# Kernel optimization log

Hardware: AMD Instinct MI355X
Metric: run time of the kernel (lower is better)

Reference implementation:

```python
import jax, jax.numpy as jnp
import numpy as np

NUM_HEADS = 8
MASK_RATE = 0.5


def setup_inputs() -> dict:
    key = jax.random.key(0)
    ks = jax.random.split(key, 6)
    B, N, C = 8, 1024, 256
    TABLE = 10
    att_embedding = jax.random.normal(ks[0], (B, N, C), dtype=jnp.float32)
    relation_position = jax.random.randint(ks[1], (B, N, N), 0, TABLE, dtype=jnp.int32)
    rel_len = jax.random.randint(ks[2], (B,), 0, 20, dtype=jnp.int32)
    W_qkv = jax.random.normal(ks[3], (C, 3 * C), dtype=jnp.float32) * (1.0 / np.sqrt(C))
    W_proj = jax.random.normal(ks[4], (C, C), dtype=jnp.float32) * (1.0 / np.sqrt(C))
    b_proj = jnp.zeros((C,), dtype=jnp.float32)
    bias_table = jax.random.normal(ks[5], (TABLE, NUM_HEADS), dtype=jnp.float32) * 0.02
    return {
        "att_embedding": att_embedding,
        "relation_position": relation_position,
        "rel_len": rel_len,
        "W_qkv": W_qkv,
        "W_proj": W_proj,
        "b_proj": b_proj,
        "bias_table": bias_table,
    }


def reference(att_embedding, relation_position, rel_len, W_qkv, W_proj, b_proj, bias_table):
    B, N, C = att_embedding.shape
    H = NUM_HEADS
    hd = C // H
    scale = hd ** -0.5

    # QKV projection (no bias): [B,N,3C] -> q,k,v each [B,H,N,hd]
    qkv = (att_embedding @ W_qkv).reshape(B, N, 3, H, hd)
    qkv = jnp.transpose(qkv, (2, 0, 3, 1, 4))
    q, k, v = qkv[0], qkv[1], qkv[2]

    # Attention scores [B,H,N,N]
    attn = jnp.einsum("bhnd,bhmd->bhnm", q, k) * scale

    # Relative position bias: gather [B,N,N,H] -> [B,H,N,N]
    pos_bias = jnp.transpose(bias_table[relation_position], (0, 3, 1, 2))

    # Mask bias: table row t gets -100 iff t > mask_len (mask_len+1 .. TABLE-1);
    # identical across heads -> compute as [B,1,N,N] instead of materializing [B,H,N,N].
    mask_len = (rel_len.astype(jnp.float32) * MASK_RATE).astype(jnp.int32)
    mask_bias = jnp.where(relation_position > mask_len[:, None, None], -100.0, 0.0)[:, None]

    attn = jax.nn.softmax(attn + pos_bias + mask_bias, axis=-1)

    # Weighted values -> [B,N,C] -> output projection
    x = jnp.einsum("bhnm,bhmd->bnhd", attn, v).reshape(B, N, C)
    x = x @ W_proj + b_proj
    return x
```

## Files before the change

### kernel.cpp

```cpp
#include <hip/hip_runtime.h>
#include <hip/hip_bf16.h>

typedef __bf16 bf16;
typedef __bf16 bf16x2 __attribute__((ext_vector_type(2)));
typedef __bf16 bf16x8 __attribute__((ext_vector_type(8)));
typedef float f32x4 __attribute__((ext_vector_type(4)));
typedef int i32x4 __attribute__((ext_vector_type(4)));

#define B_ 8
#define N_ 1024
#define C_ 256
#define H_ 8
#define C3_ 768
#define SCALE 0.17677669529663689f
#define FMAX 16.0f


__global__ __launch_bounds__(256) void prep(
    const float* __restrict__ Wqkv, const float* __restrict__ Wproj,
    bf16* __restrict__ Wq_tiled, bf16* __restrict__ Wp_tiled)
{
  int bb = blockIdx.x;
  int o = bb * 256 + threadIdx.x;
  if (bb < 768) {
    int kk = o & 31;
    int idx = o >> 5;
    int nr = idx & 63;
    int qq = idx >> 6;
    int nt = qq % 12, kt = qq / 12;
    int n = nt * 64 + nr, k = kt * 32 + kk;
    Wq_tiled[o] = (bf16)Wqkv[k * C3_ + n];
  } else {
    int p = o - 768 * 256;
    int kk = p & 31;
    int n = (p >> 5) & 255;
    int kt = p >> 13;
    int k = kt * 32 + kk;
    Wp_tiled[p] = (bf16)Wproj[k * C_ + n];
  }
}

__global__ __launch_bounds__(256) void gemm_qkv(
    const float* __restrict__ A, const bf16* __restrict__ Wq_tiled,
    bf16* __restrict__ q, bf16* __restrict__ kT, bf16* __restrict__ vT)
{
  __shared__ bf16 As[128][40];
  __shared__ bf16 Bts[128][40];
  __shared__ bf16 Vls[64][136];

  int tid = threadIdx.x;
  int wave = tid >> 6, lane = tid & 63, quad = lane >> 4, l16 = lane & 15;
  int m0 = blockIdx.x * 128, n0 = blockIdx.y * 128;
  int msub = (wave & 1) * 64, nsub = (wave >> 1) * 64;

  f32x4 acc[4][4] = {};

  int arow = tid >> 1, akc = (tid & 1) * 16;
  const float* aptr = A + (long)(m0 + arow) * C_ + akc;
  int bn = tid >> 1, bkc = (tid & 1) * 16;
  const bf16* bptr = Wq_tiled +
      ((long)(blockIdx.y * 2 + (bn >> 6)) * 2048 + (bn & 63) * 32 + bkc);

  float4 a0 = *reinterpret_cast<const float4*>(aptr);
  float4 a1 = *reinterpret_cast<const float4*>(aptr + 4);
  float4 a2 = *reinterpret_cast<const float4*>(aptr + 8);
  float4 a3 = *reinterpret_cast<const float4*>(aptr + 12);
  i32x4 bv0 = *reinterpret_cast<const i32x4*>(bptr);
  i32x4 bv1 = *reinterpret_cast<const i32x4*>(bptr + 8);

  for (int kt = 0; kt < 8; ++kt) {
    __syncthreads();
    {
      bf16 at[16] = {(bf16)a0.x, (bf16)a0.y, (bf16)a0.z, (bf16)a0.w,
                     (bf16)a1.x, (bf16)a1.y, (bf16)a1.z, (bf16)a1.w,
                     (bf16)a2.x, (bf16)a2.y, (bf16)a2.z, (bf16)a2.w,
                     (bf16)a3.x, (bf16)a3.y, (bf16)a3.z, (bf16)a3.w};
      *reinterpret_cast<bf16x8*>(&As[arow][akc]) = *reinterpret_cast<bf16x8*>(at);
      *reinterpret_cast<bf16x8*>(&As[arow][akc + 8]) = *reinterpret_cast<bf16x8*>(at + 8);
      *reinterpret_cast<i32x4*>(&Bts[bn][bkc]) = bv0;
      *reinterpret_cast<i32x4*>(&Bts[bn][bkc + 8]) = bv1;
    }
    __syncthreads();

    if (kt < 7) {
      int kn = (kt + 1) * 32;
      a0 = *reinterpret_cast<const float4*>(aptr + kn);
      a1 = *reinterpret_cast<const float4*>(aptr + kn + 4);
      a2 = *reinterpret_cast<const float4*>(aptr + kn + 8);
      a3 = *reinterpret_cast<const float4*>(aptr + kn + 12);
      bv0 = *reinterpret_cast<const i32x4*>(bptr + (long)(kt + 1) * 24576);
      bv1 = *reinterpret_cast<const i32x4*>(bptr + (long)(kt + 1) * 24576 + 8);
    }

    bf16x8 af[4], bfr[4];
#pragma unroll
    for (int mi = 0; mi < 4; ++mi)
      af[mi] = *reinterpret_cast<const bf16x8*>(&As[msub + mi * 16 + l16][quad * 8]);
#pragma unroll
    for (int ni = 0; ni < 4; ++ni)
      bfr[ni] = *reinterpret_cast<const bf16x8*>(&Bts[nsub + ni * 16 + l16][quad * 8]);
#pragma unroll
    for (int mi = 0; mi < 4; ++mi)
#pragma unroll
      for (int ni = 0; ni < 4; ++ni)
        acc[mi][ni] = __builtin_amdgcn_mfma_f32_16x16x32_bf16(af[mi], bfr[ni], acc[mi][ni], 0, 0, 0);
  }

  if (n0 < 256) {
#pragma unroll
    for (int mi = 0; mi < 4; ++mi)
#pragma unroll
      for (int ni = 0; ni < 4; ++ni)
#pragma unroll
        for (int r = 0; r < 4; ++r) {
          int row = m0 + msub + mi * 16 + quad * 4 + r;
          int col = n0 + nsub + ni * 16 + l16;
          q[(long)row * 256 + col] = (bf16)(acc[mi][ni][r] * SCALE);
        }
  } else if (n0 < 512) {
#pragma unroll
    for (int mi = 0; mi < 4; ++mi)
#pragma unroll
      for (int ni = 0; ni < 4; ++ni)
#pragma unroll
        for (int r = 0; r < 4; ++r) {
          int row = m0 + msub + mi * 16 + quad * 4 + r;
          int c = n0 + nsub + ni * 16 + l16 - 256;
          int b = row >> 10, n = row & 1023;
          int h = c >> 5, d = c & 31;
          kT[(((long)(b * H_ + h)) * N_ + n) * 32 + d] = (bf16)acc[mi][ni][r];
        }
  } else {
    int b = m0 >> 10;
#pragma unroll
    for (int ch = 0; ch < 2; ++ch) {
      __syncthreads();
      if ((nsub >> 6) == ch) {
#pragma unroll
        for (int mi = 0; mi < 4; ++mi)
#pragma unroll
          for (int ni = 0; ni < 4; ++ni)
#pragma unroll
            for (int r = 0; r < 4; ++r) {
              int cc = ni * 16 + l16;
              int nn = msub + mi * 16 + quad * 4 + r;
              int np = (nn & 96) | (2 * (nn & 15)) | ((nn >> 4) & 1);
              Vls[cc][np] = (bf16)acc[mi][ni][r];
            }
      }
      __syncthreads();
      int cc = tid >> 2, nseg = (tid & 3) * 32;
      long base = ((long)(b * C_ + (n0 - 512) + ch * 64 + cc)) * N_ + (m0 & 1023) + nseg;
#pragma unroll
      for (int j = 0; j < 4; ++j)
        *reinterpret_cast<i32x4*>(vT + base + j * 8) =
            *reinterpret_cast<const i32x4*>(&Vls[cc][nseg + j * 8]);
    }
  }
}

__global__ __launch_bounds__(512) void flash_attn(
    const bf16* __restrict__ q, const bf16* __restrict__ kT,
    const bf16* __restrict__ vT, const int* __restrict__ rel,
    const int* __restrict__ rel_len, const float* __restrict__ btab,
    const bf16* __restrict__ Wp_tiled, const float* __restrict__ bias,
    float* __restrict__ out)
{
  __shared__ bf16 Vs[256][40];
  __shared__ unsigned RelsP[4][33];
  __shared__ bf16 Pls[H_][16 * 40];
  __shared__ float btl[H_][16];
  __shared__ bf16 attL[16][264];

  int tid = threadIdx.x;
  int h = tid >> 6, lane = tid & 63, quad = lane >> 4, l16 = lane & 15;
  int b = blockIdx.y, i0 = blockIdx.x * 16;
  long bN = (long)b * N_;

  int mask_len = (int)((float)rel_len[b] * 0.5f);
  if (tid < 80) {
    int t = tid >> 3, hh = tid & 7;
    btl[hh][t] = btab[t * H_ + hh] + (t > mask_len ? -100.f : 0.f) - FMAX;
  }

  bf16x8 qf = *reinterpret_cast<const bf16x8*>(
      q + (bN + i0 + l16) * 256 + h * 32 + quad * 8);

  const bf16* kbase = kT + ((long)(b * H_ + h)) * N_ * 32 + quad * 8;
  int vrow = tid >> 1, voff = (tid & 1) * 16;
  const bf16* vgp = vT + ((long)b * C_ + vrow) * N_ + voff;
  int rg = (tid >> 5) & 3, rcol = tid & 31;
  const int* rgp = rel + (bN + i0 + rg * 4) * N_ + rcol;

  bf16x8 kf0 = *reinterpret_cast<const bf16x8*>(kbase + (long)l16 * 32);
  bf16x8 kf1 = *reinterpret_cast<const bf16x8*>(kbase + (long)(16 + l16) * 32);
  bf16x8 vr0 = *reinterpret_cast<const bf16x8*>(vgp);
  bf16x8 vr1 = *reinterpret_cast<const bf16x8*>(vgp + 8);
  int rr0 = 0, rr1 = 0, rr2 = 0, rr3 = 0;
  if (tid < 128) {
    rr0 = rgp[0]; rr1 = rgp[N_]; rr2 = rgp[2 * N_]; rr3 = rgp[3 * N_];
  }

  f32x4 oacc[2] = {};
  float l_part[4] = {0.f, 0.f, 0.f, 0.f};

  for (int j0 = 0; j0 < N_; j0 += 32) {
    __syncthreads();
    *reinterpret_cast<bf16x8*>(&Vs[vrow][voff]) = vr0;
    *reinterpret_cast<bf16x8*>(&Vs[vrow][voff + 8]) = vr1;
    if (tid < 128)
      RelsP[rg][rcol] = (unsigned)rr0 | ((unsigned)rr1 << 8) |
                        ((unsigned)rr2 << 16) | ((unsigned)rr3 << 24);
    __syncthreads();

    int jn = j0 + 32; jn = (jn < N_) ? jn : 0;
    bf16x8 kn0 = *reinterpret_cast<const bf16x8*>(kbase + (long)(jn + l16) * 32);
    bf16x8 kn1 = *reinterpret_cast<const bf16x8*>(kbase + (long)(jn + 16 + l16) * 32);
    vr0 = *reinterpret_cast<const bf16x8*>(vgp + jn);
    vr1 = *reinterpret_cast<const bf16x8*>(vgp + jn + 8);
    if (tid < 128) {
      rr0 = rgp[jn]; rr1 = rgp[N_ + jn];
      rr2 = rgp[2 * N_ + jn]; rr3 = rgp[3 * N_ + jn];
    }

    f32x4 z = {};
    f32x4 s0 = __builtin_amdgcn_mfma_f32_16x16x32_bf16(qf, kf0, z, 0, 0, 0);
    f32x4 s1 = __builtin_amdgcn_mfma_f32_16x16x32_bf16(qf, kf1, z, 0, 0, 0);
    kf0 = kn0; kf1 = kn1;

    unsigned w0 = RelsP[quad][l16];
    unsigned w1 = RelsP[quad][16 + l16];
#pragma unroll
    for (int r = 0; r < 4; ++r) {
      int il = quad * 4 + r;
      int rv0 = (w0 >> (8 * r)) & 255;
      int rv1 = (w1 >> (8 * r)) & 255;
      float p0 = __expf(s0[r] + btl[h][rv0]);
      float p1 = __expf(s1[r] + btl[h][rv1]);
      l_part[r] += p0 + p1;
      bf16x2 pp = {(bf16)p0, (bf16)p1};
      *reinterpret_cast<bf16x2*>(&Pls[h][il * 40 + l16 * 2]) = pp;
    }
    asm volatile("s_waitcnt lgkmcnt(0)" ::: "memory");
    bf16x8 pf = *reinterpret_cast<const bf16x8*>(&Pls[h][l16 * 40 + quad * 8]);
    bf16x8 vf0 = *reinterpret_cast<const bf16x8*>(&Vs[h * 32 + l16][quad * 8]);
    bf16x8 vf1 = *reinterpret_cast<const bf16x8*>(&Vs[h * 32 + 16 + l16][quad * 8]);
    oacc[0] = __builtin_amdgcn_mfma_f32_16x16x32_bf16(pf, vf0, oacc[0], 0, 0, 0);
    oacc[1] = __builtin_amdgcn_mfma_f32_16x16x32_bf16(pf, vf1, oacc[1], 0, 0, 0);
  }

#pragma unroll
  for (int r = 0; r < 4; ++r) {
    float l = l_part[r];
#pragma unroll
    for (int m = 1; m < 16; m <<= 1) l += __shfl_xor(l, m);
    float inv = 1.f / l;
    attL[quad * 4 + r][h * 32 + l16] = (bf16)(oacc[0][r] * inv);
    attL[quad * 4 + r][h * 32 + 16 + l16] = (bf16)(oacc[1][r] * inv);
  }
  __syncthreads();

  f32x4 pacc[2] = {};
  const bf16* wp = Wp_tiled + ((h * 32 + l16) * 32 + quad * 8);
#pragma unroll
  for (int kt = 0; kt < 8; ++kt) {
    bf16x8 afr = *reinterpret_cast<const bf16x8*>(&attL[l16][kt * 32 + quad * 8]);
    bf16x8 b0 = *reinterpret_cast<const bf16x8*>(wp + kt * 8192);
    bf16x8 b1 = *reinterpret_cast<const bf16x8*>(wp + kt * 8192 + 512);
    pacc[0] = __builtin_amdgcn_mfma_f32_16x16x32_bf16(afr, b0, pacc[0], 0, 0, 0);
    pacc[1] = __builtin_amdgcn_mfma_f32_16x16x32_bf16(afr, b1, pacc[1], 0, 0, 0);
  }
  float bi0 = bias[h * 32 + l16];
  float bi1 = bias[h * 32 + 16 + l16];
#pragma unroll
  for (int r = 0; r < 4; ++r) {
    long rowoff = (bN + i0 + quad * 4 + r) * C_ + h * 32;
    out[rowoff + l16] = pacc[0][r] + bi0;
    out[rowoff + 16 + l16] = pacc[1][r] + bi1;
  }
}

extern "C" void kernel_launch(void* const* d_in, const int* in_sizes, int n_in,
                              void* d_out, int out_size, void* d_ws, size_t ws_size,
                              hipStream_t stream) {
  const float* X     = (const float*)d_in[0];
  const int*   rel   = (const int*)d_in[1];
  const int*   rlen  = (const int*)d_in[2];
  const float* Wqkv  = (const float*)d_in[3];
  const float* Wproj = (const float*)d_in[4];
  const float* bproj = (const float*)d_in[5];
  const float* btab  = (const float*)d_in[6];
  float* out = (float*)d_out;

  char* ws = (char*)d_ws;
  bf16* Wq_tiled = (bf16*)ws;
  bf16* Wp_tiled = (bf16*)(ws + 393216);
  bf16* q  = (bf16*)(ws + 524288);
  bf16* kT = (bf16*)(ws + 524288 + 4194304);
  bf16* vT = (bf16*)(ws + 524288 + 2 * 4194304);

  prep<<<dim3(1024), 256, 0, stream>>>(Wqkv, Wproj, Wq_tiled, Wp_tiled);
  gemm_qkv<<<dim3(8192 / 128, C3_ / 128), 256, 0, stream>>>(X, Wq_tiled, q, kT, vT);
  flash_attn<<<dim3(N_ / 16, B_), 512, 0, stream>>>(
      q, kT, vT, rel, rlen, btab, Wp_tiled, bproj, out);
}
```

Before: 140.1 us.

## Remove block-wide barriers from attention loop via per-wave V and relation loads

Each wave now loads its own head's V slice and its own relation indices directly into registers, so both __syncthreads calls in the key loop are dropped and waves run independently. The bias table is replicated four times to reduce LDS bank conflicts and pre-scaled by log2(e), and the q scale folds in log2(e) so exp2f can replace __expf. The cost is redundant global reads of the relation indices by all eight waves instead of a shared packed copy, plus more registers. Intra-wave LDS reuse of Vs relies on lockstep execution and the lgkmcnt wait.

```diff
diff --git a/kernel.cpp b/kernel.cpp
--- a/kernel.cpp
+++ b/kernel.cpp
@@ -12,7 +12,7 @@
 #define C_ 256
 #define H_ 8
 #define C3_ 768
-#define SCALE 0.17677669529663689f
+#define QS 0.25500398f
 #define FMAX 16.0f
 
 
@@ -115,7 +115,7 @@
         for (int r = 0; r < 4; ++r) {
           int row = m0 + msub + mi * 16 + quad * 4 + r;
           int col = n0 + nsub + ni * 16 + l16;
-          q[(long)row * 256 + col] = (bf16)(acc[mi][ni][r] * SCALE);
+          q[(long)row * 256 + col] = (bf16)(acc[mi][ni][r] * QS);
         }
   } else if (n0 < 512) {
 #pragma unroll
@@ -166,10 +166,9 @@
     const bf16* __restrict__ Wp_tiled, const float* __restrict__ bias,
     float* __restrict__ out)
 {
-  __shared__ bf16 Vs[256][40];
-  __shared__ unsigned RelsP[4][33];
+  __shared__ bf16 Vs[H_][32][40];
   __shared__ bf16 Pls[H_][16 * 40];
-  __shared__ float btl[H_][16];
+  __shared__ float btlq[4][H_][17];
   __shared__ bf16 attL[16][264];
 
   int tid = threadIdx.x;
@@ -178,49 +177,49 @@
   long bN = (long)b * N_;
 
   int mask_len = (int)((float)rel_len[b] * 0.5f);
-  if (tid < 80) {
-    int t = tid >> 3, hh = tid & 7;
-    btl[hh][t] = btab[t * H_ + hh] + (t > mask_len ? -100.f : 0.f) - FMAX;
-  }
+  if (tid < 320) {
+    int cp = tid / 80, rem = tid % 80, t = rem >> 3, hh = rem & 7;
+    btlq[cp][hh][t] =
+        (btab[t * H_ + hh] + (t > mask_len ? -100.f : 0.f) - FMAX) * 1.44269504f;
+  }
+  __syncthreads();
 
   bf16x8 qf = *reinterpret_cast<const bf16x8*>(
       q + (bN + i0 + l16) * 256 + h * 32 + quad * 8);
 
   const bf16* kbase = kT + ((long)(b * H_ + h)) * N_ * 32 + quad * 8;
-  int vrow = tid >> 1, voff = (tid & 1) * 16;
-  const bf16* vgp = vT + ((long)b * C_ + vrow) * N_ + voff;
-  int rg = (tid >> 5) & 3, rcol = tid & 31;
-  const int* rgp = rel + (bN + i0 + rg * 4) * N_ + rcol;
+  int vrl = lane >> 1, voff = (lane & 1) * 16;
+  const bf16* vgp = vT + ((long)b * C_ + h * 32 + vrl) * N_ + voff;
+  const int* relr = rel + (bN + i0 + quad * 4) * N_ + l16;
 
   bf16x8 kf0 = *reinterpret_cast<const bf16x8*>(kbase + (long)l16 * 32);
   bf16x8 kf1 = *reinterpret_cast<const bf16x8*>(kbase + (long)(16 + l16) * 32);
   bf16x8 vr0 = *reinterpret_cast<const bf16x8*>(vgp);
   bf16x8 vr1 = *reinterpret_cast<const bf16x8*>(vgp + 8);
-  int rr0 = 0, rr1 = 0, rr2 = 0, rr3 = 0;
-  if (tid < 128) {
-    rr0 = rgp[0]; rr1 = rgp[N_]; rr2 = rgp[2 * N_]; rr3 = rgp[3 * N_];
+  int rv[8];
+#pragma unroll
+  for (int r = 0; r < 4; ++r) {
+    rv[r] = relr[(long)r * N_];
+    rv[4 + r] = relr[(long)r * N_ + 16];
   }
 
   f32x4 oacc[2] = {};
   float l_part[4] = {0.f, 0.f, 0.f, 0.f};
 
   for (int j0 = 0; j0 < N_; j0 += 32) {
-    __syncthreads();
-    *reinterpret_cast<bf16x8*>(&Vs[vrow][voff]) = vr0;
-    *reinterpret_cast<bf16x8*>(&Vs[vrow][voff + 8]) = vr1;
-    if (tid < 128)
-      RelsP[rg][rcol] = (unsigned)rr0 | ((unsigned)rr1 << 8) |
-                        ((unsigned)rr2 << 16) | ((unsigned)rr3 << 24);
-    __syncthreads();
+    *reinterpret_cast<bf16x8*>(&Vs[h][vrl][voff]) = vr0;
+    *reinterpret_cast<bf16x8*>(&Vs[h][vrl][voff + 8]) = vr1;
 
     int jn = j0 + 32; jn = (jn < N_) ? jn : 0;
     bf16x8 kn0 = *reinterpret_cast<const bf16x8*>(kbase + (long)(jn + l16) * 32);
     bf16x8 kn1 = *reinterpret_cast<const bf16x8*>(kbase + (long)(jn + 16 + l16) * 32);
-    vr0 = *reinterpret_cast<const bf16x8*>(vgp + jn);
-    vr1 = *reinterpret_cast<const bf16x8*>(vgp + jn + 8);
-    if (tid < 128) {
-      rr0 = rgp[jn]; rr1 = rgp[N_ + jn];
-      rr2 = rgp[2 * N_ + jn]; rr3 = rgp[3 * N_ + jn];
+    bf16x8 vn0 = *reinterpret_cast<const bf16x8*>(vgp + jn);
+    bf16x8 vn1 = *reinterpret_cast<const bf16x8*>(vgp + jn + 8);
+    int rn[8];
+#pragma unroll
+    for (int r = 0; r < 4; ++r) {
+      rn[r] = relr[(long)r * N_ + jn];
+      rn[4 + r] = relr[(long)r * N_ + jn + 16];
     }
 
     f32x4 z = {};
@@ -228,25 +227,26 @@
     f32x4 s1 = __builtin_amdgcn_mfma_f32_16x16x32_bf16(qf, kf1, z, 0, 0, 0);
     kf0 = kn0; kf1 = kn1;
 
-    unsigned w0 = RelsP[quad][l16];
-    unsigned w1 = RelsP[quad][16 + l16];
 #pragma unroll
     for (int r = 0; r < 4; ++r) {
       int il = quad * 4 + r;
-      int rv0 = (w0 >> (8 * r)) & 255;
-      int rv1 = (w1 >> (8 * r)) & 255;
-      float p0 = __expf(s0[r] + btl[h][rv0]);
-      float p1 = __expf(s1[r] + btl[h][rv1]);
+      float p0 = exp2f(s0[r] + btlq[quad][h][rv[r]]);
+      float p1 = exp2f(s1[r] + btlq[quad][h][rv[4 + r]]);
       l_part[r] += p0 + p1;
       bf16x2 pp = {(bf16)p0, (bf16)p1};
       *reinterpret_cast<bf16x2*>(&Pls[h][il * 40 + l16 * 2]) = pp;
     }
+#pragma unroll
+    for (int t = 0; t < 8; ++t) rv[t] = rn[t];
+
     asm volatile("s_waitcnt lgkmcnt(0)" ::: "memory");
     bf16x8 pf = *reinterpret_cast<const bf16x8*>(&Pls[h][l16 * 40 + quad * 8]);
-    bf16x8 vf0 = *reinterpret_cast<const bf16x8*>(&Vs[h * 32 + l16][quad * 8]);
-    bf16x8 vf1 = *reinterpret_cast<const bf16x8*>(&Vs[h * 32 + 16 + l16][quad * 8]);
+    bf16x8 vf0 = *reinterpret_cast<const bf16x8*>(&Vs[h][l16][quad * 8]);
+    bf16x8 vf1 = *reinterpret_cast<const bf16x8*>(&Vs[h][16 + l16][quad * 8]);
     oacc[0] = __builtin_amdgcn_mfma_f32_16x16x32_bf16(pf, vf0, oacc[0], 0, 0, 0);
     oacc[1] = __builtin_amdgcn_mfma_f32_16x16x32_bf16(pf, vf1, oacc[1], 0, 0, 0);
+
+    vr0 = vn0; vr1 = vn1;
   }
 
 #pragma unroll
```

New measurement: 152.8 us. 9.0% more time.
